# Performance work log

Measured on AMD Instinct MI355X. Metric: run time of the kernel, lower is better.

## Reference

```python
import jax, jax.numpy as jnp
import numpy as np
from jax import lax

S, B = 2048, 2048          # seq_len, batch (seq-first layout like nn.LSTM)
IN, H, OUT, L = 2, 4, 1, 4  # from module defaults


def setup_inputs() -> dict:
    key = jax.random.key(0)
    ks = jax.random.split(key, 11)
    s = 0.5  # ~ PyTorch init scale 1/sqrt(H)
    return {
        "x": jax.random.normal(ks[0], (S, B, IN), jnp.float32),
        "W_ih0": jax.random.normal(ks[1], (4 * H, IN), jnp.float32) * s,
        "W_hh0": jax.random.normal(ks[2], (4 * H, H), jnp.float32) * s,
        "b_ih0": jax.random.normal(ks[3], (4 * H,), jnp.float32) * s,
        "b_hh0": jax.random.normal(ks[4], (4 * H,), jnp.float32) * s,
        "W_ihr": jax.random.normal(ks[5], (L - 1, 4 * H, H), jnp.float32) * s,
        "W_hhr": jax.random.normal(ks[6], (L - 1, 4 * H, H), jnp.float32) * s,
        "b_ihr": jax.random.normal(ks[7], (L - 1, 4 * H), jnp.float32) * s,
        "b_hhr": jax.random.normal(ks[8], (L - 1, 4 * H), jnp.float32) * s,
        "W_out": jax.random.normal(ks[9], (OUT, H), jnp.float32) * s,
        "b_out": jax.random.normal(ks[10], (OUT,), jnp.float32) * s,
    }


def _lstm_layer(x, Wih, Whh, b):
    # x: [S, B, D_in]; PyTorch gate order: i, f, g, o
    Bsz = x.shape[1]
    Hh = Whh.shape[1]
    # precompute input contribution for all timesteps (batched GEMM)
    xg = jnp.einsum('sbd,gd->sbg', x, Wih) + b  # [S, B, 4H]

    def step(carry, xgt):
        h, c = carry
        gates = xgt + h @ Whh.T  # [B, 4H]
        i, f, g, o = jnp.split(gates, 4, axis=-1)
        c = jax.nn.sigmoid(f) * c + jax.nn.sigmoid(i) * jnp.tanh(g)
        h = jax.nn.sigmoid(o) * jnp.tanh(c)
        return (h, c), h

    init = (jnp.zeros((Bsz, Hh), x.dtype), jnp.zeros((Bsz, Hh), x.dtype))
    _, ys = lax.scan(step, init, xg)
    return ys  # [S, B, H]


def reference(x, W_ih0, W_hh0, b_ih0, b_hh0, W_ihr, W_hhr, b_ihr, b_hhr, W_out, b_out):
    h = _lstm_layer(x, W_ih0, W_hh0, b_ih0 + b_hh0)
    for l in range(W_ihr.shape[0]):  # fixed small layer loop
        h = _lstm_layer(h, W_ihr[l], W_hhr[l], b_ihr[l] + b_hhr[l])
    # dropout: identity in eval mode (deterministic reference)
    y = jnp.einsum('sbh,oh->sbo', h, W_out) + b_out  # linear head, [S, B, 1]
    return y
```

## Files before the change

### kernel.cpp

```cpp
#include <hip/hip_runtime.h>

#define S_LEN 2048
#define B_SZ 2048

typedef float v2 __attribute__((ext_vector_type(2)));
#define FMA2(a, b, c) __builtin_elementwise_fma((a), (b), (c))

template <int CTRL>
__device__ __forceinline__ float dppmov(float v) {
  int r = __builtin_amdgcn_update_dpp(0, __builtin_bit_cast(int, v), CTRL, 0xF,
                                      0xF, true);
  return __builtin_bit_cast(float, r);
}

#define TICK(U)                                                                \
  {                                                                            \
    float4 nhin = *(const float4 *)(&Rf[(((U) + 7) & 7) * 80 + rd_off]);       \
    v2 h01, h23;                                                               \
    h01.x = hin.x;                                                             \
    h01.y = hin.y;                                                             \
    h23.x = hin.z;                                                             \
    h23.y = hin.w;                                                             \
    v2 A0 = FMA2(wi01[0], h01, bias2[0]);                                      \
    v2 A1 = FMA2(wi01[1], h01, bias2[1]);                                      \
    v2 A2 = FMA2(wi01[2], h01, bias2[2]);                                      \
    v2 A3 = FMA2(wi01[3], h01, bias2[3]);                                      \
    A0 = FMA2(wi23[0], h23, A0);                                               \
    A1 = FMA2(wi23[1], h23, A1);                                               \
    A2 = FMA2(wi23[2], h23, A2);                                               \
    A3 = FMA2(wi23[3], h23, A3);                                               \
    A0 = FMA2(wh01[0], hv01, A0);                                              \
    A1 = FMA2(wh01[1], hv01, A1);                                              \
    A2 = FMA2(wh01[2], hv01, A2);                                              \
    A3 = FMA2(wh01[3], hv01, A3);                                              \
    A0 = FMA2(wh23[0], hv23, A0);                                              \
    A1 = FMA2(wh23[1], hv23, A1);                                              \
    A2 = FMA2(wh23[2], hv23, A2);                                              \
    A3 = FMA2(wh23[3], hv23, A3);                                              \
    float a0 = A0.x + A0.y, a1 = A1.x + A1.y;                                  \
    float a2 = A2.x + A2.y, a3 = A3.x + A3.y;                                  \
    float e0 = __builtin_amdgcn_exp2f(a0);       \
    float e1 = __builtin_amdgcn_exp2f(a1);                                     \
    float e2 = __builtin_amdgcn_exp2f(a2);                                     \
    float e3 = __builtin_amdgcn_exp2f(a3);                                     \
    float r0 = __builtin_amdgcn_rcpf(1.0f + e0);               \
    float r1 = __builtin_amdgcn_rcpf(1.0f + e1);               \
    float r2 = __builtin_amdgcn_rcpf(1.0f + e2);            \
    float r3 = __builtin_amdgcn_rcpf(1.0f + e3);               \
    float gi = KT * r0;                               \
    float gg = fmaf(2.0f, r2, -1.0f);                             \
    cKT = fmaf(r1, cKT, gi * gg);                                              \
    float te = __builtin_amdgcn_exp2f(cKT);                                    \
    float tr = __builtin_amdgcn_rcpf(1.0f + te);                               \
    float go2 = r3 + r3;                                                       \
    float hh = fmaf(go2, tr, -r3);                          \
    Rf[(U) * 80 + wr_off] = hh;                                                \
    hv01.x = hh;                                                               \
    hv01.y = dppmov<0x39>(hh);                                \
    hv23.x = dppmov<0x4E>(hh);                                \
    hv23.y = dppmov<0x93>(hh);                                \
    hin = nhin;                                                                \
  }

#define RESET(U)                                                               \
  if (2 * l > (U)) {                                                           \
    cKT = 0.0f;                                                                \
    hv01.x = 0.0f;                                                             \
    hv01.y = 0.0f;                                                             \
    hv23.x = 0.0f;                                                             \
    hv23.y = 0.0f;                                                             \
  }

#define PREFETCH()                                                             \
  {                                                                            \
    int ci = xi < ximax ? xi : ximax;                                          \
    gx = px[ci];                                                               \
    xi += 8 * B_SZ;                                                            \
  }

#define REFILL_Y()                                                             \
  {                                                                            \
    *(float2 *)(&Rf[xw_off]) = gx;                                             \
    float4 h4 = *(const float4 *)(&Rf[r8 * 80 + 48 + bq * 4]);                 \
    float yv = fmaf(                                                           \
        wo3, h4.w,                                                             \
        fmaf(wo2, h4.z, fmaf(wo1, h4.y, fmaf(wo0, h4.x, bo))));                \
    if (lane < 32 && (unsigned)yi < (unsigned)(S_LEN * B_SZ)) outp[yi] = yv;   \
    yi += 8 * B_SZ;                                                            \
  }

__global__ void __launch_bounds__(64, 1)
    lstm_kernel(const float *__restrict__ x, const float *__restrict__ Wih0,
                const float *__restrict__ Whh0, const float *__restrict__ bih0,
                const float *__restrict__ bhh0, const float *__restrict__ Wihr,
                const float *__restrict__ Whhr, const float *__restrict__ bihr,
                const float *__restrict__ bhhr, const float *__restrict__ Wout,
                const float *__restrict__ bout, float *__restrict__ out) {
  __shared__ __align__(16) float Rf[704];

  const int lane = threadIdx.x & 63;
  const int b = lane >> 4;
  const int l = (lane >> 2) & 3;
  const int j = lane & 3;
  const int bidx = blockIdx.x * 4 + b;
  const int r8 = lane & 7;
  const int bq = (lane >> 3) & 3;
  const int colq = blockIdx.x * 4 + bq;
  const int rd_off = (l == 0) ? (64 + b * 4) : ((l - 1) * 16 + b * 4);
  const int wr_off = l * 16 + b * 4 + j;
  const int xw_off =
      (lane < 32) ? (r8 * 80 + 64 + bq * 4) : (640 + (lane - 32) * 2);

#pragma unroll
  for (int k = 0; k < 11; ++k) Rf[lane + 64 * k] = 0.0f;
  __builtin_amdgcn_wave_barrier();

  const float L2E = 1.4426950408889634f;
  const float KT = -2.8853900817779268f;
  const float kks[4] = {-L2E, -L2E, -2.0f * L2E, -L2E};

  v2 wi01[4], wi23[4], wh01[4], wh23[4], bias2[4];
#pragma unroll
  for (int t = 0; t < 4; ++t) {
    const int row = t * 4 + j;
    const float kk = kks[t];
    float i0, i1, i2, i3, w0, w1, w2, w3, bs;
    if (l == 0) {
      i0 = Wih0[row * 2 + 0];
      i1 = Wih0[row * 2 + 1];
      i2 = 0.0f;
      i3 = 0.0f;
      w0 = Whh0[row * 4 + j];
      w1 = Whh0[row * 4 + ((j + 1) & 3)];
      w2 = Whh0[row * 4 + ((j + 2) & 3)];
      w3 = Whh0[row * 4 + ((j + 3) & 3)];
      bs = bih0[row] + bhh0[row];
    } else {
      const int m = l - 1;
      i0 = Wihr[m * 64 + row * 4 + 0];
      i1 = Wihr[m * 64 + row * 4 + 1];
      i2 = Wihr[m * 64 + row * 4 + 2];
      i3 = Wihr[m * 64 + row * 4 + 3];
      w0 = Whhr[m * 64 + row * 4 + j];
      w1 = Whhr[m * 64 + row * 4 + ((j + 1) & 3)];
      w2 = Whhr[m * 64 + row * 4 + ((j + 2) & 3)];
      w3 = Whhr[m * 64 + row * 4 + ((j + 3) & 3)];
      bs = bihr[m * 16 + row] + bhhr[m * 16 + row];
    }
    wi01[t].x = kk * i0;
    wi01[t].y = kk * i1;
    wi23[t].x = kk * i2;
    wi23[t].y = kk * i3;
    wh01[t].x = kk * w0;
    wh01[t].y = kk * w1;
    wh23[t].x = kk * w2;
    wh23[t].y = kk * w3;
    bias2[t].x = kk * bs;
    bias2[t].y = 0.0f;
  }
  const float wo0 = Wout[0], wo1 = Wout[1], wo2 = Wout[2], wo3 = Wout[3];
  const float bo = bout[0];

  v2 hv01, hv23;
  hv01.x = 0.0f;
  hv01.y = 0.0f;
  hv23.x = 0.0f;
  hv23.y = 0.0f;
  float cKT = 0.0f;
  float4 hin;

  const float2 *__restrict__ px = (const float2 *)x;
  float *__restrict__ outp = out;

  {
    float2 xz = px[bidx];
    hin.x = (l == 0) ? xz.x : 0.0f;
    hin.y = (l == 0) ? xz.y : 0.0f;
    hin.z = 0.0f;
    hin.w = 0.0f;
  }

  {
    int tp = 1 + ((r8 + 1) & 7);
    float2 xv = px[tp * B_SZ + colq];
    *(float2 *)(&Rf[xw_off]) = xv;
  }
  __builtin_amdgcn_wave_barrier();

  int xi = (9 + ((r8 + 1) & 7)) * B_SZ + colq;
  const int ximax = (S_LEN - 1) * B_SZ + colq;
  int yi = (r8 - 6) * B_SZ + colq;
  float2 gx;

  PREFETCH();
  TICK(0); RESET(0);
  TICK(1); RESET(1);
  TICK(2); RESET(2);
  TICK(3); RESET(3);
  TICK(4); RESET(4);
  TICK(5); RESET(5);
  TICK(6);
  TICK(7);
  REFILL_Y();

  for (int k = 1; k < 257; ++k) {
    PREFETCH();
    TICK(0);
    TICK(1);
    TICK(2);
    TICK(3);
    TICK(4);
    TICK(5);
    TICK(6);
    TICK(7);
    REFILL_Y();
  }
}

extern "C" void kernel_launch(void *const *d_in, const int *in_sizes, int n_in,
                              void *d_out, int out_size, void *d_ws,
                              size_t ws_size, hipStream_t stream) {
  (void)in_sizes;
  (void)n_in;
  (void)out_size;
  (void)d_ws;
  (void)ws_size;
  const float *x = (const float *)d_in[0];
  const float *Wih0 = (const float *)d_in[1];
  const float *Whh0 = (const float *)d_in[2];
  const float *bih0 = (const float *)d_in[3];
  const float *bhh0 = (const float *)d_in[4];
  const float *Wihr = (const float *)d_in[5];
  const float *Whhr = (const float *)d_in[6];
  const float *bihr = (const float *)d_in[7];
  const float *bhhr = (const float *)d_in[8];
  const float *Wout = (const float *)d_in[9];
  const float *bout = (const float *)d_in[10];
  lstm_kernel<<<dim3(B_SZ / 4), dim3(64), 0, stream>>>(
      x, Wih0, Whh0, bih0, bhh0, Wihr, Whhr, bihr, bhhr, Wout, bout,
      (float *)d_out);
}
```

Before: 377.6 us.

## Pass hidden state between layers with DPP row shifts instead of LDS

Removes the LDS ring buffer that carried each layer's hidden output to the next layer. A DPP row-shift moves the h vector from the lane group of layer l to that of layer l+1, and layer-0 lanes now load x directly into an eight-deep register queue. The output head is computed in every tick by the layer-3 lanes and stored straight to global memory, with the input weights rotated to match the DPP ordering. This takes LDS writes, reads and their latency off the serial recurrence path, at the cost of more per-tick global loads and stores and more registers.

```diff
diff --git a/kernel.cpp b/kernel.cpp
--- a/kernel.cpp
+++ b/kernel.cpp
@@ -15,12 +15,16 @@
 
 #define TICK(U)                                                                \
   {                                                                            \
-    float4 nhin = *(const float4 *)(&Rf[(((U) + 7) & 7) * 80 + rd_off]);       \
+                \
+    float s0 = dppmov<0x114>(hv01.x);                           \
+    float s1 = dppmov<0x114>(hv01.y);                                          \
+    float s2 = dppmov<0x114>(hv23.x);                                          \
+    float s3 = dppmov<0x114>(hv23.y);                                          \
     v2 h01, h23;                                                               \
-    h01.x = hin.x;                                                             \
-    h01.y = hin.y;                                                             \
-    h23.x = hin.z;                                                             \
-    h23.y = hin.w;                                                             \
+    h01.x = hx0;                                                               \
+    h01.y = hx1;                                                               \
+    h23.x = hx2;                                                               \
+    h23.y = hx3;                                                               \
     v2 A0 = FMA2(wi01[0], h01, bias2[0]);                                      \
     v2 A1 = FMA2(wi01[1], h01, bias2[1]);                                      \
     v2 A2 = FMA2(wi01[2], h01, bias2[2]);                                      \
@@ -54,12 +58,23 @@
     float tr = __builtin_amdgcn_rcpf(1.0f + te);                               \
     float go2 = r3 + r3;                                                       \
     float hh = fmaf(go2, tr, -r3);                          \
-    Rf[(U) * 80 + wr_off] = hh;                                                \
     hv01.x = hh;                                                               \
     hv01.y = dppmov<0x39>(hh);                                \
     hv23.x = dppmov<0x4E>(hh);                                \
     hv23.y = dppmov<0x93>(hh);                                \
-    hin = nhin;                                                                \
+           \
+           \
+    hx0 = lz ? xc##U.x : s0;                                                   \
+    hx1 = lz ? xc##U.y : s1;                                                   \
+    hx2 = s2;                                                                  \
+    hx3 = s3;                                                                  \
+             \
+    float yv = fmaf(wo3, hv23.y,                                               \
+                    fmaf(wo2, hv23.x, fmaf(wo1, hv01.y, fmaf(wo0, hv01.x,      \
+                                                             bo))));           \
+    if (yl && (unsigned)ty < (unsigned)S_LEN) outp[yi] = yv;                   \
+    ty += 1;                                                                   \
+    yi += B_SZ;                                                                \
   }
 
 #define RESET(U)                                                               \
@@ -71,22 +86,11 @@
     hv23.y = 0.0f;                                                             \
   }
 
-#define PREFETCH()                                                             \
+#define XLOAD(U, TB)                                                           \
   {                                                                            \
-    int ci = xi < ximax ? xi : ximax;                                          \
-    gx = px[ci];                                                               \
-    xi += 8 * B_SZ;                                                            \
-  }
-
-#define REFILL_Y()                                                             \
-  {                                                                            \
-    *(float2 *)(&Rf[xw_off]) = gx;                                             \
-    float4 h4 = *(const float4 *)(&Rf[r8 * 80 + 48 + bq * 4]);                 \
-    float yv = fmaf(                                                           \
-        wo3, h4.w,                                                             \
-        fmaf(wo2, h4.z, fmaf(wo1, h4.y, fmaf(wo0, h4.x, bo))));                \
-    if (lane < 32 && (unsigned)yi < (unsigned)(S_LEN * B_SZ)) outp[yi] = yv;   \
-    yi += 8 * B_SZ;                                                            \
+    int t_ = (TB) + (U);                                                       \
+    if (t_ >= S_LEN) t_ = S_LEN - 1;          \
+    xc##U = px[(size_t)t_ * B_SZ + bidx];                                      \
   }
 
 __global__ void __launch_bounds__(64, 1)
@@ -96,24 +100,13 @@
                 const float *__restrict__ Whhr, const float *__restrict__ bihr,
                 const float *__restrict__ bhhr, const float *__restrict__ Wout,
                 const float *__restrict__ bout, float *__restrict__ out) {
-  __shared__ __align__(16) float Rf[704];
-
   const int lane = threadIdx.x & 63;
   const int b = lane >> 4;
   const int l = (lane >> 2) & 3;
   const int j = lane & 3;
   const int bidx = blockIdx.x * 4 + b;
-  const int r8 = lane & 7;
-  const int bq = (lane >> 3) & 3;
-  const int colq = blockIdx.x * 4 + bq;
-  const int rd_off = (l == 0) ? (64 + b * 4) : ((l - 1) * 16 + b * 4);
-  const int wr_off = l * 16 + b * 4 + j;
-  const int xw_off =
-      (lane < 32) ? (r8 * 80 + 64 + bq * 4) : (640 + (lane - 32) * 2);
-
-#pragma unroll
-  for (int k = 0; k < 11; ++k) Rf[lane + 64 * k] = 0.0f;
-  __builtin_amdgcn_wave_barrier();
+  const bool lz = (l == 0);
+  const bool yl = (l == 3) && (j == 0);
 
   const float L2E = 1.4426950408889634f;
   const float KT = -2.8853900817779268f;
@@ -137,10 +130,10 @@
       bs = bih0[row] + bhh0[row];
     } else {
       const int m = l - 1;
-      i0 = Wihr[m * 64 + row * 4 + 0];
-      i1 = Wihr[m * 64 + row * 4 + 1];
-      i2 = Wihr[m * 64 + row * 4 + 2];
-      i3 = Wihr[m * 64 + row * 4 + 3];
+      i0 = Wihr[m * 64 + row * 4 + j];
+      i1 = Wihr[m * 64 + row * 4 + ((j + 1) & 3)];
+      i2 = Wihr[m * 64 + row * 4 + ((j + 2) & 3)];
+      i3 = Wihr[m * 64 + row * 4 + ((j + 3) & 3)];
       w0 = Whhr[m * 64 + row * 4 + j];
       w1 = Whhr[m * 64 + row * 4 + ((j + 1) & 3)];
       w2 = Whhr[m * 64 + row * 4 + ((j + 2) & 3)];
@@ -161,59 +154,57 @@
   const float wo0 = Wout[0], wo1 = Wout[1], wo2 = Wout[2], wo3 = Wout[3];
   const float bo = bout[0];
 
+  const float2 *__restrict__ px = (const float2 *)x;
+  float *__restrict__ outp = out;
+
   v2 hv01, hv23;
   hv01.x = 0.0f;
   hv01.y = 0.0f;
   hv23.x = 0.0f;
   hv23.y = 0.0f;
   float cKT = 0.0f;
-  float4 hin;
-
-  const float2 *__restrict__ px = (const float2 *)x;
-  float *__restrict__ outp = out;
+  float hx0, hx1, hx2, hx3;
 
   {
-    float2 xz = px[bidx];
-    hin.x = (l == 0) ? xz.x : 0.0f;
-    hin.y = (l == 0) ? xz.y : 0.0f;
-    hin.z = 0.0f;
-    hin.w = 0.0f;
-  }
-
-  {
-    int tp = 1 + ((r8 + 1) & 7);
-    float2 xv = px[tp * B_SZ + colq];
-    *(float2 *)(&Rf[xw_off]) = xv;
-  }
-  __builtin_amdgcn_wave_barrier();
-
-  int xi = (9 + ((r8 + 1) & 7)) * B_SZ + colq;
-  const int ximax = (S_LEN - 1) * B_SZ + colq;
-  int yi = (r8 - 6) * B_SZ + colq;
-  float2 gx;
-
-  PREFETCH();
-  TICK(0); RESET(0);
-  TICK(1); RESET(1);
-  TICK(2); RESET(2);
-  TICK(3); RESET(3);
-  TICK(4); RESET(4);
-  TICK(5); RESET(5);
-  TICK(6);
-  TICK(7);
-  REFILL_Y();
-
+    float2 x00 = px[bidx];
+    hx0 = lz ? x00.x : 0.0f;
+    hx1 = lz ? x00.y : 0.0f;
+    hx2 = 0.0f;
+    hx3 = 0.0f;
+  }
+
+  float2 xc0 = px[1 * B_SZ + bidx];
+  float2 xc1 = px[2 * B_SZ + bidx];
+  float2 xc2 = px[3 * B_SZ + bidx];
+  float2 xc3 = px[4 * B_SZ + bidx];
+  float2 xc4 = px[5 * B_SZ + bidx];
+  float2 xc5 = px[6 * B_SZ + bidx];
+  float2 xc6 = px[7 * B_SZ + bidx];
+  float2 xc7 = px[8 * B_SZ + bidx];
+
+  int ty = -6;
+  int yi = -6 * B_SZ + bidx;
+
+  TICK(0); RESET(0); XLOAD(0, 9);
+  TICK(1); RESET(1); XLOAD(1, 9);
+  TICK(2); RESET(2); XLOAD(2, 9);
+  TICK(3); RESET(3); XLOAD(3, 9);
+  TICK(4); RESET(4); XLOAD(4, 9);
+  TICK(5); RESET(5); XLOAD(5, 9);
+  TICK(6); XLOAD(6, 9);
+  TICK(7); XLOAD(7, 9);
+
+#pragma unroll 1
   for (int k = 1; k < 257; ++k) {
-    PREFETCH();
-    TICK(0);
-    TICK(1);
-    TICK(2);
-    TICK(3);
-    TICK(4);
-    TICK(5);
-    TICK(6);
-    TICK(7);
-    REFILL_Y();
+    const int tb = 8 * k + 9;
+    TICK(0); XLOAD(0, tb);
+    TICK(1); XLOAD(1, tb);
+    TICK(2); XLOAD(2, tb);
+    TICK(3); XLOAD(3, tb);
+    TICK(4); XLOAD(4, tb);
+    TICK(5); XLOAD(5, tb);
+    TICK(6); XLOAD(6, tb);
+    TICK(7); XLOAD(7, tb);
   }
 }
 
```

After: 437.3 us. +15.8%, slower.
